# Performance work log

Measured on AMD Instinct MI355X. Metric: run time of the kernel, lower is better.

Reference implementation:

```python
import jax, jax.numpy as jnp
import numpy as np

EMBED_DIM = 768
NUM_HEADS = 12
HEAD_DIM = EMBED_DIM // NUM_HEADS // 2  # 32
MLP_DIM = 3072
DEPTH = 1
LAMBDA_INIT = 0.8 - 0.6 * float(np.exp(-0.3 * (DEPTH - 1)))  # 0.2
EPS = 1e-5


def layernorm(x, g, b):
    mu = jnp.mean(x, axis=-1, keepdims=True)
    var = jnp.mean((x - mu) ** 2, axis=-1, keepdims=True)
    return (x - mu) * jax.lax.rsqrt(var + EPS) * g + b


def rmsnorm(x, g):
    ms = jnp.mean(x ** 2, axis=-1, keepdims=True)
    return x * jax.lax.rsqrt(ms + EPS) * g


def setup_inputs() -> dict:
    key = jax.random.key(0)
    ks = jax.random.split(key, 16)
    d, m, hd = EMBED_DIM, MLP_DIM, HEAD_DIM
    inp = {
        "x": jax.random.normal(ks[0], (32, 577, d), dtype=jnp.float32),
        "ln1_g": jnp.ones((d,), jnp.float32),
        "ln1_b": jnp.zeros((d,), jnp.float32),
        "wq": jax.random.normal(ks[1], (d, d), jnp.float32) * 0.02,
        "wk": jax.random.normal(ks[2], (d, d), jnp.float32) * 0.02,
        "wv": jax.random.normal(ks[3], (d, d), jnp.float32) * 0.02,
        "wo": jax.random.normal(ks[4], (d, d), jnp.float32) * 0.02,
        "lq1": jax.random.normal(ks[5], (hd,), jnp.float32) * 0.1,
        "lk1": jax.random.normal(ks[6], (hd,), jnp.float32) * 0.1,
        "lq2": jax.random.normal(ks[7], (hd,), jnp.float32) * 0.1,
        "lk2": jax.random.normal(ks[8], (hd,), jnp.float32) * 0.1,
        "subln_g": jnp.ones((2 * hd,), jnp.float32),
        "ln2_g": jnp.ones((d,), jnp.float32),
        "ln2_b": jnp.zeros((d,), jnp.float32),
        "w1": jax.random.normal(ks[9], (m, d), jnp.float32) * 0.02,
        "b1": jnp.zeros((m,), jnp.float32),
        "w2": jax.random.normal(ks[10], (d, m), jnp.float32) * 0.02,
        "b2": jnp.zeros((d,), jnp.float32),
    }
    return inp


def diff_attn(x, wq, wk, wv, wo, lq1, lk1, lq2, lk2, subln_g):
    b, n, d = x.shape
    h, hd = NUM_HEADS, HEAD_DIM
    q = (x @ wq.T).reshape(b, n, 2 * h, hd)  # [b,n,2h,hd]
    k = (x @ wk.T).reshape(b, n, 2 * h, hd)
    v = (x @ wv.T).reshape(b, n, h, 2 * hd)  # [b,n,h,2hd]
    scale = hd ** -0.5
    scores = jnp.einsum("bnhd,bmhd->bhnm", q * scale, k)  # [b,2h,n,n]
    probs = jax.nn.softmax(scores.astype(jnp.float32), axis=-1).astype(x.dtype)
    probs = probs.reshape(b, h, 2, n, n)
    lam = jnp.exp(jnp.sum(lq1 * lk1)) - jnp.exp(jnp.sum(lq2 * lk2)) + LAMBDA_INIT
    attn = probs[:, :, 0] - lam * probs[:, :, 1]  # [b,h,n,n]
    out = jnp.einsum("bhnm,bmhe->bnhe", attn, v)  # [b,n,h,2hd]
    out = rmsnorm(out, subln_g) * (1.0 - LAMBDA_INIT)
    return out.reshape(b, n, d) @ wo.T


def reference(x, ln1_g, ln1_b, wq, wk, wv, wo, lq1, lk1, lq2, lk2, subln_g,
              ln2_g, ln2_b, w1, b1, w2, b2):
    # pre-LN -> differential attention -> residual
    a = diff_attn(layernorm(x, ln1_g, ln1_b), wq, wk, wv, wo,
                  lq1, lk1, lq2, lk2, subln_g)
    x = x + a
    # pre-LN -> GELU MLP -> residual (dropout = 0 / eval)
    h = layernorm(x, ln2_g, ln2_b)
    h = jax.nn.gelu(h @ w1.T + b1, approximate=False) @ w2.T + b2
    return x + h
```

## Files before the change

kernel.cpp:

```cpp
#include <hip/hip_runtime.h>
#include <hip/hip_bf16.h>
#include <cstdint>
#include <cstddef>

typedef __bf16 bf16_t;
typedef __attribute__((ext_vector_type(8))) __bf16 bf16x8;
typedef __attribute__((ext_vector_type(4))) __bf16 bf16x4;
typedef __attribute__((ext_vector_type(4))) float f32x4;
typedef __attribute__((ext_vector_type(4))) int int4v;
typedef __attribute__((ext_vector_type(2))) unsigned uintx2;

#define DEV static __device__ __forceinline__

#define BATCH 32
#define SEQ 577
#define DMODEL 768
#define MROWS (BATCH * SEQ)
#define MPAD 18688
#define NH 12
#define HDIM 32
#define EDIM 64
#define MLPD 3072
#define NPAD 640
#define QKVSTR 2304

DEV f32x4 mfma16(bf16x8 a, bf16x8 b, f32x4 c) {
    return __builtin_amdgcn_mfma_f32_16x16x32_bf16(a, b, c, 0, 0, 0);
}

DEV void gload16(const void* g, void* l) {
    __builtin_amdgcn_global_load_lds(
        (const __attribute__((address_space(1))) void*)(uintptr_t)g,
        (__attribute__((address_space(3))) void*)(uintptr_t)l,
        16, 0, 0);
}

DEV unsigned cvt_pk_bf16(float lo, float hi) {
    unsigned r;
    asm("v_cvt_pk_bf16_f32 %0, %1, %2" : "=v"(r) : "v"(lo), "v"(hi));
    return r;
}
DEV void plane16_swap(unsigned& a, unsigned& b) {
    asm("v_permlane16_swap_b32 %0, %1" : "+v"(a), "+v"(b));
}
DEV void plane32_swap(unsigned& a, unsigned& b) {
    asm("v_permlane32_swap_b32 %0, %1" : "+v"(a), "+v"(b));
}

DEV int xcd_swz(int orig, int nwg) {
    const int q = nwg >> 3, r = nwg & 7;
    const int xcd = orig & 7, loc = orig >> 3;
    return (xcd < r ? xcd * (q + 1) : r * (q + 1) + (xcd - r) * q) + loc;
}

__global__ __launch_bounds__(256)
void wconv_kernel(const float* __restrict__ wq, const float* __restrict__ wk,
                  const float* __restrict__ wv, const float* __restrict__ wo,
                  const float* __restrict__ w1, const float* __restrict__ w2,
                  bf16_t* __restrict__ dst)
{
    const size_t idx = ((size_t)blockIdx.x * 256 + threadIdx.x) * 4;
    const float* src;
    size_t off;
    if      (idx <  589824) { src = wq; off = idx; }
    else if (idx < 1179648) { src = wk; off = idx - 589824; }
    else if (idx < 1769472) { src = wv; off = idx - 1179648; }
    else if (idx < 2359296) { src = wo; off = idx - 1769472; }
    else if (idx < 4718592) { src = w1; off = idx - 2359296; }
    else                    { src = w2; off = idx - 4718592; }
    const f32x4 v = *(const f32x4*)&src[off];
    bf16x4 o;
#pragma unroll
    for (int u = 0; u < 4; ++u) o[u] = (bf16_t)v[u];
    *(bf16x4*)&dst[idx] = o;
}

__global__ void lam_kernel(const float* __restrict__ lq1, const float* __restrict__ lk1,
                           const float* __restrict__ lq2, const float* __restrict__ lk2,
                           float* __restrict__ lam)
{
    const int l = threadIdx.x;
    float a = 0.f, c = 0.f;
    if (l < 32) { a = lq1[l] * lk1[l]; c = lq2[l] * lk2[l]; }
#pragma unroll
    for (int m = 1; m < 32; m <<= 1) { a += __shfl_xor(a, m); c += __shfl_xor(c, m); }
    if (l == 0) *lam = expf(a) - expf(c) + 0.2f;
}

__global__ __launch_bounds__(256)
void ln_kernel(const float* __restrict__ src, const float* __restrict__ g,
               const float* __restrict__ bt, bf16_t* __restrict__ dst, const int Mv)
{
    const int row = blockIdx.x;
    const int t = threadIdx.x;
    if (row >= Mv) {
        for (int i = t; i < DMODEL; i += 256) dst[(size_t)row * DMODEL + i] = (bf16_t)0.f;
        return;
    }
    const float* p = src + (size_t)row * DMODEL;
    const float v0 = p[t], v1 = p[t + 256], v2 = p[t + 512];
    float s = v0 + v1 + v2, s2 = v0 * v0 + v1 * v1 + v2 * v2;
#pragma unroll
    for (int m = 1; m < 64; m <<= 1) { s += __shfl_xor(s, m); s2 += __shfl_xor(s2, m); }
    __shared__ float red[8];
    const int w = t >> 6;
    if ((t & 63) == 0) { red[w] = s; red[4 + w] = s2; }
    __syncthreads();
    s  = red[0] + red[1] + red[2] + red[3];
    s2 = red[4] + red[5] + red[6] + red[7];
    const float mu  = s * (1.f / DMODEL);
    const float var = s2 * (1.f / DMODEL) - mu * mu;
    const float rs = rsqrtf(var + 1e-5f);
    bf16_t* d = dst + (size_t)row * DMODEL;
    d[t      ] = (bf16_t)((v0 - mu) * rs * g[t      ] + bt[t      ]);
    d[t + 256] = (bf16_t)((v1 - mu) * rs * g[t + 256] + bt[t + 256]);
    d[t + 512] = (bf16_t)((v2 - mu) * rs * g[t + 512] + bt[t + 512]);
}

#define VM6 asm volatile("s_waitcnt vmcnt(6)" ::: "memory")
#define VM4 asm volatile("s_waitcnt vmcnt(4)" ::: "memory")
#define VM2 asm volatile("s_waitcnt vmcnt(2)" ::: "memory")
#define VM0 asm volatile("s_waitcnt vmcnt(0)" ::: "memory")
#define RAWBAR do { __builtin_amdgcn_s_barrier(); \
                    __builtin_amdgcn_sched_barrier(0); } while (0)

#define QUAD(MH, NH)                                                         \
    do {                                                                     \
        __builtin_amdgcn_s_setprio(1);                                       \
        _Pragma("unroll")                                                    \
        for (int m2_ = 0; m2_ < 4; ++m2_)                                    \
            _Pragma("unroll")                                                \
            for (int n2_ = 0; n2_ < 2; ++n2_)                                \
                _Pragma("unroll")                                            \
                for (int ks_ = 0; ks_ < 2; ++ks_)                            \
                    acc[(MH) * 4 + m2_][(NH) * 2 + n2_] =                    \
                        mfma16(af[m2_][ks_], bfr[n2_][ks_],                  \
                               acc[(MH) * 4 + m2_][(NH) * 2 + n2_]);         \
        __builtin_amdgcn_s_setprio(0);                                       \
    } while (0)

template <int EPI>
__global__ __launch_bounds__(512, 2)
void gemm8(const bf16_t* __restrict__ A, const bf16_t* __restrict__ W,
           const int K, const int N, const int NT,
           bf16_t* __restrict__ outB, float* __restrict__ outF,
           const float* __restrict__ bias, const float* __restrict__ resid,
           const int Mv)
{
    __shared__ bf16_t As[2][256 * 64];
    __shared__ bf16_t Bs[2][256 * 64];
    const int t = threadIdx.x;
    const int l = t & 63, w = t >> 6;
    const int lg = l >> 4, lc = l & 15;
    const int wr = w >> 2, wc = w & 3;

    const int nwg = gridDim.x * gridDim.y;
    const int orig = blockIdx.y * gridDim.x + blockIdx.x;
    const int wg = xcd_swz(orig, nwg);
    const int tileRow = (wg / gridDim.y) * 256;
    const int tileCol = (wg % gridDim.y) * 256;

    const int srow = t >> 3;
    const int swc = ((t & 7) ^ (srow & 7)) * 8;
    const bf16_t* pA0 = A + (size_t)(tileRow + srow) * K + swc;
    const bf16_t* pB0 = W + (size_t)(tileCol + srow) * K + swc;
    const size_t rstep = (size_t)64 * K;

    f32x4 acc[8][4];
#pragma unroll
    for (int m = 0; m < 8; ++m)
#pragma unroll
        for (int n = 0; n < 4; ++n) acc[m][n] = f32x4{0.f, 0.f, 0.f, 0.f};

    auto stA = [&](int bsel, int tk, int mh) {
        const bf16_t* s = pA0 + (size_t)tk * 64 + (size_t)mh * 128 * K;
        gload16(s,         &As[bsel][(mh * 1024 + t) * 8]);
        gload16(s + rstep, &As[bsel][(mh * 1024 + 512 + t) * 8]);
    };
    auto stB = [&](int bsel, int tk, int nh) {
        const bf16_t* s = pB0 + (size_t)tk * 64 + (size_t)nh * 128 * K;
        gload16(s,         &Bs[bsel][(nh * 1024 + t) * 8]);
        gload16(s + rstep, &Bs[bsel][(nh * 1024 + 512 + t) * 8]);
    };

    bf16x8 af[4][2], bfr[2][2];
    const int rdsw = lc & 7;
    auto rdA = [&](int bsel, int mh) {
#pragma unroll
        for (int m2 = 0; m2 < 4; ++m2)
#pragma unroll
            for (int ks = 0; ks < 2; ++ks)
                af[m2][ks] = *(const bf16x8*)&As[bsel][
                    (mh * 128 + m2 * 32 + wr * 16 + lc) * 64 + ((ks * 4 + lg) ^ rdsw) * 8];
    };
    auto rdB = [&](int bsel, int nh) {
#pragma unroll
        for (int n2 = 0; n2 < 2; ++n2)
#pragma unroll
            for (int ks = 0; ks < 2; ++ks)
                bfr[n2][ks] = *(const bf16x8*)&Bs[bsel][
                    (nh * 128 + n2 * 64 + wc * 16 + lc) * 64 + ((ks * 4 + lg) ^ rdsw) * 8];
    };

    stA(0, 0, 0);
    stB(0, 0, 0);
    stB(0, 0, 1);
    stA(0, 0, 1);

#pragma unroll 1
    for (int kt = 0; kt < NT - 1; ++kt) {
        const int bs = kt & 1, bn = bs ^ 1;
        stA(bn, kt + 1, 0); VM6; RAWBAR;
        rdA(bs, 0); rdB(bs, 0); QUAD(0, 0);
        stB(bn, kt + 1, 0); VM6; RAWBAR;
        rdB(bs, 1); QUAD(0, 1);
        stB(bn, kt + 1, 1); VM6; RAWBAR;
        rdA(bs, 1); QUAD(1, 1);
        stA(bn, kt + 1, 1);
        rdB(bs, 0); QUAD(1, 0);
    }
    {
        const int bs = (NT - 1) & 1;
        VM4; RAWBAR;
        rdA(bs, 0); rdB(bs, 0); QUAD(0, 0);
        VM2; RAWBAR;
        rdB(bs, 1); QUAD(0, 1);
        VM0; RAWBAR;
        rdA(bs, 1); QUAD(1, 1);
        rdB(bs, 0); QUAD(1, 0);
    }

#pragma unroll
    for (int m = 0; m < 8; ++m) {
        const int row0 = tileRow + (m >> 2) * 128 + (m & 3) * 32 + wr * 16 + 4 * lg;
#pragma unroll
        for (int n = 0; n < 4; ++n) {
            const int col = tileCol + (n >> 1) * 128 + (n & 1) * 64 + wc * 16 + lc;
#pragma unroll
            for (int r = 0; r < 4; ++r) {
                const int row = row0 + r;
                float v = acc[m][n][r];
                if (EPI == 0) {
                    outB[(size_t)row * N + col] = (bf16_t)v;
                } else if (EPI == 1) {
                    const float xin = (row < Mv) ? resid[(size_t)row * N + col] : 0.f;
                    outF[(size_t)row * N + col] = v + xin;
                } else if (EPI == 2) {
                    v += bias[col];
                    v = 0.5f * v * (1.f + erff(v * 0.70710678118654752f));
                    outB[(size_t)row * N + col] = (bf16_t)v;
                } else {
                    if (row < Mv)
                        outF[(size_t)row * N + col] = v + bias[col] + resid[(size_t)row * N + col];
                }
            }
        }
    }
}

__global__ __launch_bounds__(256)
void vtrans_kernel(const bf16_t* __restrict__ qkv, bf16_t* __restrict__ vt)
{
    const int nt = blockIdx.x, h = blockIdx.y, b = blockIdx.z;
    const int t = threadIdx.x;
    __shared__ bf16_t T[64][72];
    {
        const int nl = t >> 2, e0 = (t & 3) * 16;
        const int n = nt * 64 + nl;
        bf16x8 a, c;
        if (n < SEQ) {
            const bf16_t* src = &qkv[((size_t)b * SEQ + n) * QKVSTR + 1536 + h * EDIM + e0];
            a = *(const bf16x8*)src;
            c = *(const bf16x8*)(src + 8);
        } else {
#pragma unroll
            for (int u = 0; u < 8; ++u) { a[u] = (bf16_t)0.f; c[u] = (bf16_t)0.f; }
        }
#pragma unroll
        for (int u = 0; u < 8; ++u) { T[e0 + u][nl] = a[u]; T[e0 + 8 + u][nl] = c[u]; }
    }
    __syncthreads();
    {
        const int e = t >> 2, n0 = (t & 3) * 16;
        bf16x8 a, c;
#pragma unroll
        for (int u = 0; u < 8; ++u) { a[u] = T[e][n0 + u]; c[u] = T[e][n0 + 8 + u]; }
        bf16_t* d = &vt[((size_t)(b * NH + h) * EDIM + e) * NPAD + nt * 64 + n0];
        *(bf16x8*)d = a;
        *(bf16x8*)(d + 8) = c;
    }
}

__global__ __launch_bounds__(256)
void attn_kernel(const bf16_t* __restrict__ qkv, const bf16_t* __restrict__ vtp,
                 const float* __restrict__ lamp, const float* __restrict__ subg,
                 bf16_t* __restrict__ outp)
{
    const int orig = blockIdx.x + 10 * (blockIdx.y + 12 * blockIdx.z);
    const int wg = xcd_swz(orig, 3840);
    const int qt = wg % 10;
    const int h  = (wg / 10) % 12;
    const int b  = wg / 120;
    const int t = threadIdx.x, w = t >> 6, l = t & 63;
    const int lg = l >> 4, lc = l & 15;
    const float lam = *lamp;
    const float SC2 = 0.25503487f;
    const float MARG = 8.0f * 0.25503487f;

    __shared__ bf16_t Ks[2][64 * 64];
    __shared__ bf16_t Vs[2][64 * 64];

    const size_t mb = (size_t)b * SEQ;
    const int q0row = qt * 64 + w * 16;

    bf16x8 qf[2];
#pragma unroll
    for (int hh = 0; hh < 2; ++hh)
        qf[hh] = *(const bf16x8*)&qkv[(mb + q0row + lc) * QKVSTR
                                      + h * 64 + hh * 32 + 8 * lg];

    f32x4 O[2][4];
    f32x4 Ol[2];
#pragma unroll
    for (int hh = 0; hh < 2; ++hh) {
        Ol[hh] = f32x4{0.f, 0.f, 0.f, 0.f};
#pragma unroll
        for (int ef = 0; ef < 4; ++ef) O[hh][ef] = f32x4{0.f, 0.f, 0.f, 0.f};
    }

    bf16x8 ones;
#pragma unroll
    for (int u = 0; u < 8; ++u) ones[u] = (bf16_t)1.0f;

    const int r0 = t >> 3, c0 = (t & 7);
    const int r1 = r0 + 32;
    const bf16_t* kg0 = &qkv[(mb + r0) * QKVSTR + 768 + h * 64 + ((c0 ^ (r0 & 7)) * 8)];
    const bf16_t* kg1 = &qkv[(mb + r1) * QKVSTR + 768 + h * 64 + ((c0 ^ (r1 & 7)) * 8)];
    const bf16_t* vg0 = &vtp[(size_t)((b * NH + h) * EDIM + r0) * NPAD + ((c0 ^ (r0 & 7)) * 8)];
    const bf16_t* vg1 = &vtp[(size_t)((b * NH + h) * EDIM + r1) * NPAD + ((c0 ^ (r1 & 7)) * 8)];

    auto stage = [&](int kt, int bufi) {
        gload16(kg0 + (size_t)kt * (64 * QKVSTR), &Ks[bufi][t * 8]);
        gload16(kg1 + (size_t)kt * (64 * QKVSTR), &Ks[bufi][(t + 256) * 8]);
        gload16(vg0 + kt * 64, &Vs[bufi][t * 8]);
        gload16(vg1 + kt * 64, &Vs[bufi][(t + 256) * 8]);
    };

    stage(0, 0);
    int buf = 0;

    const int swz = lc & 7;
    int koff[2], voff[2];
#pragma unroll
    for (int hh = 0; hh < 2; ++hh) koff[hh] = lc * 64 + (((hh * 4 + lg) ^ swz) * 8);
#pragma unroll
    for (int ks = 0; ks < 2; ++ks) voff[ks] = lc * 64 + (((ks * 4 + lg) ^ swz) * 8);

#pragma unroll 1
    for (int kt = 0; kt < 10; ++kt) {
        __builtin_amdgcn_s_barrier();
        if (kt < 9) {
            stage(kt + 1, buf ^ 1);
            VM4;
        } else {
            VM0;
        }
        __builtin_amdgcn_s_barrier();
        __builtin_amdgcn_sched_barrier(0);

        const bf16_t* Kb = &Ks[buf][0];
        const bf16_t* Vb = &Vs[buf][0];

#pragma unroll
        for (int hh = 0; hh < 2; ++hh) {
            bf16x8 kf[4];
#pragma unroll
            for (int f = 0; f < 4; ++f)
                kf[f] = *(const bf16x8*)&Kb[koff[hh] + f * 1024];
            f32x4 s[4];
#pragma unroll
            for (int f = 0; f < 4; ++f)
                s[f] = mfma16(kf[f], qf[hh], f32x4{0.f, 0.f, 0.f, 0.f});
            if (kt == 9) {
#pragma unroll
                for (int f = 0; f < 4; ++f)
#pragma unroll
                    for (int r = 0; r < 4; ++r)
                        if (f | r) s[f][r] = -3e38f;
                if (lg != 0) s[0][0] = -3e38f;
            }
            unsigned wd[4][2];
#pragma unroll
            for (int f = 0; f < 4; ++f) {
                float p0 = __builtin_amdgcn_exp2f(__builtin_fmaf(s[f][0], SC2, -MARG));
                float p1 = __builtin_amdgcn_exp2f(__builtin_fmaf(s[f][1], SC2, -MARG));
                float p2 = __builtin_amdgcn_exp2f(__builtin_fmaf(s[f][2], SC2, -MARG));
                float p3 = __builtin_amdgcn_exp2f(__builtin_fmaf(s[f][3], SC2, -MARG));
                wd[f][0] = cvt_pk_bf16(p0, p1);
                wd[f][1] = cvt_pk_bf16(p2, p3);
            }
#pragma unroll
            for (int half = 0; half < 2; ++half) {
#pragma unroll
                for (int p = 0; p < 2; ++p) {
                    unsigned& Aa = wd[half * 2][p];
                    unsigned& Bb = wd[half * 2 + 1][p];
                    plane32_swap(Aa, Bb);
                    plane16_swap(Aa, Bb);
                }
            }
            const bf16x8 pa0 = __builtin_bit_cast(bf16x8,
                int4v{(int)wd[0][0], (int)wd[0][1], (int)wd[1][0], (int)wd[1][1]});
            const bf16x8 pa1 = __builtin_bit_cast(bf16x8,
                int4v{(int)wd[2][0], (int)wd[2][1], (int)wd[3][0], (int)wd[3][1]});

#pragma unroll
            for (int ef = 0; ef < 4; ++ef) {
                const bf16x8 vb0 = *(const bf16x8*)&Vb[voff[0] + ef * 1024];
                const bf16x8 vb1 = *(const bf16x8*)&Vb[voff[1] + ef * 1024];
                O[hh][ef] = mfma16(vb0, pa0, O[hh][ef]);
                O[hh][ef] = mfma16(vb1, pa1, O[hh][ef]);
            }
            Ol[hh] = mfma16(ones, pa0, Ol[hh]);
            Ol[hh] = mfma16(ones, pa1, Ol[hh]);
        }
        buf ^= 1;
    }

    {
        const float i0 = 1.f / Ol[0][0];
        const float i1 = lam / Ol[1][0];
        float comb[4][4];
        float ms = 0.f;
#pragma unroll
        for (int ef = 0; ef < 4; ++ef)
#pragma unroll
            for (int r = 0; r < 4; ++r) {
                const float o = O[0][ef][r] * i0 - O[1][ef][r] * i1;
                comb[ef][r] = o;
                ms += o * o;
            }
        ms += __shfl_xor(ms, 16);
        ms += __shfl_xor(ms, 32);
        const float sc = rsqrtf(ms * (1.f / 64.f) + 1e-5f) * 0.8f;
        const int nq = q0row + lc;
        if (nq < SEQ) {
            bf16_t* dst = &outp[(mb + nq) * DMODEL + h * EDIM + 4 * lg];
#pragma unroll
            for (int ef = 0; ef < 4; ++ef) {
                const f32x4 g4 = *(const f32x4*)&subg[ef * 16 + 4 * lg];
                const unsigned u0 = cvt_pk_bf16(comb[ef][0] * sc * g4[0],
                                                comb[ef][1] * sc * g4[1]);
                const unsigned u1 = cvt_pk_bf16(comb[ef][2] * sc * g4[2],
                                                comb[ef][3] * sc * g4[3]);
                *(uintx2*)(dst + ef * 16) = uintx2{u0, u1};
            }
        }
    }
}

extern "C" void kernel_launch(void* const* d_in, const int* in_sizes, int n_in,
                              void* d_out, int out_size, void* d_ws, size_t ws_size,
                              hipStream_t stream)
{
    const float* x    = (const float*)d_in[0];
    const float* ln1g = (const float*)d_in[1];
    const float* ln1b = (const float*)d_in[2];
    const float* wq   = (const float*)d_in[3];
    const float* wk   = (const float*)d_in[4];
    const float* wv   = (const float*)d_in[5];
    const float* wo   = (const float*)d_in[6];
    const float* lq1  = (const float*)d_in[7];
    const float* lk1  = (const float*)d_in[8];
    const float* lq2  = (const float*)d_in[9];
    const float* lk2  = (const float*)d_in[10];
    const float* subg = (const float*)d_in[11];
    const float* ln2g = (const float*)d_in[12];
    const float* ln2b = (const float*)d_in[13];
    const float* w1   = (const float*)d_in[14];
    const float* b1   = (const float*)d_in[15];
    const float* w2   = (const float*)d_in[16];
    const float* b2   = (const float*)d_in[17];

    char* ws = (char*)d_ws;
    bf16_t* wAll = (bf16_t*)ws;
    bf16_t* wob = wAll + 1769472;
    bf16_t* w1b = wAll + 2359296;
    bf16_t* w2b = wAll + 4718592;
    ws += 7077888ull * 2;
    float* lamP = (float*)ws; ws += 256;
    bf16_t* xn   = (bf16_t*)ws; ws += (size_t)MPAD * DMODEL * 2;
    bf16_t* qkvb = (bf16_t*)ws;
    bf16_t* h1   = qkvb;
    ws += (size_t)MPAD * QKVSTR * 2;
    bf16_t* vtb  = (bf16_t*)ws; ws += (size_t)(BATCH * NH) * EDIM * NPAD * 2;
    bf16_t* aout = (bf16_t*)ws; ws += (size_t)MPAD * DMODEL * 2;
    float* x1    = (float*)ws;  ws += (size_t)MPAD * DMODEL * 4;

    wconv_kernel<<<6912, 256, 0, stream>>>(wq, wk, wv, wo, w1, w2, wAll);
    lam_kernel<<<1, 64, 0, stream>>>(lq1, lk1, lq2, lk2, lamP);
    ln_kernel<<<MPAD, 256, 0, stream>>>(x, ln1g, ln1b, xn, MROWS);

    gemm8<0><<<dim3(73, 9), 512, 0, stream>>>(xn, wAll, 768, QKVSTR, 12,
                                              qkvb, nullptr, nullptr, nullptr, MROWS);

    vtrans_kernel<<<dim3(10, 12, 32), 256, 0, stream>>>(qkvb, vtb);
    attn_kernel<<<dim3(10, 12, 32), 256, 0, stream>>>(qkvb, vtb, lamP, subg, aout);

    gemm8<1><<<dim3(73, 3), 512, 0, stream>>>(aout, wob, 768, 768, 12,
                                              nullptr, x1, nullptr, x, MROWS);
    ln_kernel<<<MPAD, 256, 0, stream>>>(x1, ln2g, ln2b, xn, MROWS);
    gemm8<2><<<dim3(73, 12), 512, 0, stream>>>(xn, w1b, 768, MLPD, 12,
                                               h1, nullptr, b1, nullptr, MROWS);
    gemm8<3><<<dim3(73, 3), 512, 0, stream>>>(h1, w2b, MLPD, 768, 48,
                                              nullptr, (float*)d_out, b2, x1, MROWS);
}
```

Measured before the change: 604.0 us.

## Restructure GEMM main loop into 8-wave ping-pong schedule with separate B fragment registers

The GEMM k-loop is rescheduled so LDS fragment reads and the next tile's global loads are issued before a barrier, then MFMA quads run between barriers, in a ping-pong style. B fragments are split into two register sets (b0r, b1r) so the first-half B fragment can be reused for the last quad without re-reading LDS. The cost targeted is LDS read latency and redundant B reads exposed before MFMAs. In exchange it adds more barriers per iteration and more register pressure, which may hurt occupancy at launch bounds 512x2.

Result: no change. 600.9 us (-0.5%).

```diff
diff --git a/kernel.cpp b/kernel.cpp
--- a/kernel.cpp
+++ b/kernel.cpp
@@ -117,14 +117,13 @@
     d[t + 512] = (bf16_t)((v2 - mu) * rs * g[t + 512] + bt[t + 512]);
 }
 
-#define VM6 asm volatile("s_waitcnt vmcnt(6)" ::: "memory")
 #define VM4 asm volatile("s_waitcnt vmcnt(4)" ::: "memory")
 #define VM2 asm volatile("s_waitcnt vmcnt(2)" ::: "memory")
 #define VM0 asm volatile("s_waitcnt vmcnt(0)" ::: "memory")
-#define RAWBAR do { __builtin_amdgcn_s_barrier(); \
-                    __builtin_amdgcn_sched_barrier(0); } while (0)
-
-#define QUAD(MH, NH)                                                         \
+#define SB0 __builtin_amdgcn_sched_barrier(0)
+#define BAR __builtin_amdgcn_s_barrier()
+
+#define QUAD(MH, BFR, NHh)                                                   \
     do {                                                                     \
         __builtin_amdgcn_s_setprio(1);                                       \
         _Pragma("unroll")                                                    \
@@ -133,9 +132,9 @@
             for (int n2_ = 0; n2_ < 2; ++n2_)                                \
                 _Pragma("unroll")                                            \
                 for (int ks_ = 0; ks_ < 2; ++ks_)                            \
-                    acc[(MH) * 4 + m2_][(NH) * 2 + n2_] =                    \
-                        mfma16(af[m2_][ks_], bfr[n2_][ks_],                  \
-                               acc[(MH) * 4 + m2_][(NH) * 2 + n2_]);         \
+                    acc[(MH) * 4 + m2_][(NHh) * 2 + n2_] =                   \
+                        mfma16(af[m2_][ks_], BFR[n2_][ks_],                  \
+                               acc[(MH) * 4 + m2_][(NHh) * 2 + n2_]);        \
         __builtin_amdgcn_s_setprio(0);                                       \
     } while (0)
 
@@ -183,7 +182,7 @@
         gload16(s + rstep, &Bs[bsel][(nh * 1024 + 512 + t) * 8]);
     };
 
-    bf16x8 af[4][2], bfr[2][2];
+    bf16x8 af[4][2], b0r[2][2], b1r[2][2];
     const int rdsw = lc & 7;
     auto rdA = [&](int bsel, int mh) {
 #pragma unroll
@@ -193,41 +192,67 @@
                 af[m2][ks] = *(const bf16x8*)&As[bsel][
                     (mh * 128 + m2 * 32 + wr * 16 + lc) * 64 + ((ks * 4 + lg) ^ rdsw) * 8];
     };
-    auto rdB = [&](int bsel, int nh) {
+    auto rdB0 = [&](int bsel) {
 #pragma unroll
         for (int n2 = 0; n2 < 2; ++n2)
 #pragma unroll
             for (int ks = 0; ks < 2; ++ks)
-                bfr[n2][ks] = *(const bf16x8*)&Bs[bsel][
-                    (nh * 128 + n2 * 64 + wc * 16 + lc) * 64 + ((ks * 4 + lg) ^ rdsw) * 8];
+                b0r[n2][ks] = *(const bf16x8*)&Bs[bsel][
+                    (n2 * 64 + wc * 16 + lc) * 64 + ((ks * 4 + lg) ^ rdsw) * 8];
+    };
+    auto rdB1 = [&](int bsel) {
+#pragma unroll
+        for (int n2 = 0; n2 < 2; ++n2)
+#pragma unroll
+            for (int ks = 0; ks < 2; ++ks)
+                b1r[n2][ks] = *(const bf16x8*)&Bs[bsel][
+                    (128 + n2 * 64 + wc * 16 + lc) * 64 + ((ks * 4 + lg) ^ rdsw) * 8];
     };
 
     stA(0, 0, 0);
     stB(0, 0, 0);
     stB(0, 0, 1);
     stA(0, 0, 1);
+    VM4; BAR;
 
 #pragma unroll 1
     for (int kt = 0; kt < NT - 1; ++kt) {
         const int bs = kt & 1, bn = bs ^ 1;
-        stA(bn, kt + 1, 0); VM6; RAWBAR;
-        rdA(bs, 0); rdB(bs, 0); QUAD(0, 0);
-        stB(bn, kt + 1, 0); VM6; RAWBAR;
-        rdB(bs, 1); QUAD(0, 1);
-        stB(bn, kt + 1, 1); VM6; RAWBAR;
-        rdA(bs, 1); QUAD(1, 1);
+        rdA(bs, 0); rdB0(bs);
+        stA(bn, kt + 1, 0);
+        SB0; VM4; BAR; SB0;
+        QUAD(0, b0r, 0);
+        BAR;
+        rdB1(bs);
+        stB(bn, kt + 1, 0);
+        SB0; VM4; BAR; SB0;
+        QUAD(0, b1r, 1);
+        BAR;
+        rdA(bs, 1);
+        stB(bn, kt + 1, 1);
+        SB0; BAR; SB0;
+        QUAD(1, b1r, 1);
+        BAR;
         stA(bn, kt + 1, 1);
-        rdB(bs, 0); QUAD(1, 0);
-    }
+        SB0; VM4; BAR; SB0;
+        QUAD(1, b0r, 0);
+        BAR;
+    }
+
     {
         const int bs = (NT - 1) & 1;
-        VM4; RAWBAR;
-        rdA(bs, 0); rdB(bs, 0); QUAD(0, 0);
-        VM2; RAWBAR;
-        rdB(bs, 1); QUAD(0, 1);
-        VM0; RAWBAR;
-        rdA(bs, 1); QUAD(1, 1);
-        rdB(bs, 0); QUAD(1, 0);
+        rdA(bs, 0); rdB0(bs);
+        SB0; VM2; BAR; SB0;
+        QUAD(0, b0r, 0);
+        BAR;
+        rdB1(bs);
+        SB0; VM0; BAR; SB0;
+        QUAD(0, b1r, 1);
+        BAR;
+        rdA(bs, 1);
+        SB0; BAR; SB0;
+        QUAD(1, b1r, 1);
+        QUAD(1, b0r, 0);
     }
 
 #pragma unroll
```

## Replace 256x256 GEMM with 128x256 tile, K=32 triple-buffered pipeline

Applied to the files above, without the earlier changes.

The GEMM kernel moves from 256x256 tiles with K=64 double buffering to 128x256 tiles with K=32 and a three-stage LDS ring. Loads for step k+2 are issued while computing step k, and launch bounds allow four blocks per CU instead of two. The smaller tiles double the grid and raise occupancy, which should hide memory latency better and reduce wave quantization. In exchange, each tile reuses its operands less, so global and LDS traffic per FLOP rises and more barriers run per K step.

Measured after the change: 559.1 us. 7.4% less time.

```diff
diff --git a/kernel.cpp b/kernel.cpp
--- a/kernel.cpp
+++ b/kernel.cpp
@@ -117,38 +117,36 @@
     d[t + 512] = (bf16_t)((v2 - mu) * rs * g[t + 512] + bt[t + 512]);
 }
 
-#define VM6 asm volatile("s_waitcnt vmcnt(6)" ::: "memory")
-#define VM4 asm volatile("s_waitcnt vmcnt(4)" ::: "memory")
-#define VM2 asm volatile("s_waitcnt vmcnt(2)" ::: "memory")
+#define VM3 asm volatile("s_waitcnt vmcnt(3)" ::: "memory")
 #define VM0 asm volatile("s_waitcnt vmcnt(0)" ::: "memory")
-#define RAWBAR do { __builtin_amdgcn_s_barrier(); \
-                    __builtin_amdgcn_sched_barrier(0); } while (0)
-
-#define QUAD(MH, NH)                                                         \
+#define SB0 __builtin_amdgcn_sched_barrier(0)
+#define BAR __builtin_amdgcn_s_barrier()
+
+#define ASZ 4096
+#define BSZ 8192
+
+#define QUAD8(H, BP)                                                         \
     do {                                                                     \
         __builtin_amdgcn_s_setprio(1);                                       \
         _Pragma("unroll")                                                    \
         for (int m2_ = 0; m2_ < 4; ++m2_)                                    \
             _Pragma("unroll")                                                \
-            for (int n2_ = 0; n2_ < 2; ++n2_)                                \
-                _Pragma("unroll")                                            \
-                for (int ks_ = 0; ks_ < 2; ++ks_)                            \
-                    acc[(MH) * 4 + m2_][(NH) * 2 + n2_] =                    \
-                        mfma16(af[m2_][ks_], bfr[n2_][ks_],                  \
-                               acc[(MH) * 4 + m2_][(NH) * 2 + n2_]);         \
+            for (int j_ = 0; j_ < 2; ++j_)                                   \
+                acc[m2_][(H) * 2 + j_] =                                     \
+                    mfma16(af[m2_], BP[j_], acc[m2_][(H) * 2 + j_]);         \
         __builtin_amdgcn_s_setprio(0);                                       \
     } while (0)
 
 template <int EPI>
-__global__ __launch_bounds__(512, 2)
-void gemm8(const bf16_t* __restrict__ A, const bf16_t* __restrict__ W,
+__global__ __launch_bounds__(512, 4)
+void gemm4(const bf16_t* __restrict__ A, const bf16_t* __restrict__ W,
            const int K, const int N, const int NT,
            bf16_t* __restrict__ outB, float* __restrict__ outF,
            const float* __restrict__ bias, const float* __restrict__ resid,
            const int Mv)
 {
-    __shared__ bf16_t As[2][256 * 64];
-    __shared__ bf16_t Bs[2][256 * 64];
+    __shared__ bf16_t As[3 * ASZ];
+    __shared__ bf16_t Bs[3 * BSZ];
     const int t = threadIdx.x;
     const int l = t & 63, w = t >> 6;
     const int lg = l >> 4, lc = l & 15;
@@ -157,85 +155,77 @@
     const int nwg = gridDim.x * gridDim.y;
     const int orig = blockIdx.y * gridDim.x + blockIdx.x;
     const int wg = xcd_swz(orig, nwg);
-    const int tileRow = (wg / gridDim.y) * 256;
+    const int tileRow = (wg / gridDim.y) * 128;
     const int tileCol = (wg % gridDim.y) * 256;
 
-    const int srow = t >> 3;
-    const int swc = ((t & 7) ^ (srow & 7)) * 8;
-    const bf16_t* pA0 = A + (size_t)(tileRow + srow) * K + swc;
-    const bf16_t* pB0 = W + (size_t)(tileCol + srow) * K + swc;
-    const size_t rstep = (size_t)64 * K;
-
-    f32x4 acc[8][4];
-#pragma unroll
-    for (int m = 0; m < 8; ++m)
+    const int srow = t >> 2;
+    const int csrc = ((t & 3) ^ ((t >> 3) & 3)) * 8;
+    const bf16_t* srcA  = A + (size_t)(tileRow + srow) * K + csrc;
+    const bf16_t* srcB0 = W + (size_t)(tileCol + srow) * K + csrc;
+    const bf16_t* srcB1 = W + (size_t)(tileCol + 128 + srow) * K + csrc;
+
+    f32x4 acc[4][4];
+#pragma unroll
+    for (int m = 0; m < 4; ++m)
 #pragma unroll
         for (int n = 0; n < 4; ++n) acc[m][n] = f32x4{0.f, 0.f, 0.f, 0.f};
 
-    auto stA = [&](int bsel, int tk, int mh) {
-        const bf16_t* s = pA0 + (size_t)tk * 64 + (size_t)mh * 128 * K;
-        gload16(s,         &As[bsel][(mh * 1024 + t) * 8]);
-        gload16(s + rstep, &As[bsel][(mh * 1024 + 512 + t) * 8]);
+    const int rch = (lg ^ ((lc >> 1) & 3)) * 8;
+    const int aoff = (wr * 64 + lc) * 32 + rch;
+    const int boff = (wc * 64 + lc) * 32 + rch;
+
+    bf16x8 af[4], b01[2], b23[2];
+
+    auto stageA = [&](int kt, bf16_t* dst) {
+        gload16(srcA + (size_t)kt * 32, dst + t * 8);
     };
-    auto stB = [&](int bsel, int tk, int nh) {
-        const bf16_t* s = pB0 + (size_t)tk * 64 + (size_t)nh * 128 * K;
-        gload16(s,         &Bs[bsel][(nh * 1024 + t) * 8]);
-        gload16(s + rstep, &Bs[bsel][(nh * 1024 + 512 + t) * 8]);
+    auto stageB = [&](int kt, bf16_t* dst) {
+        gload16(srcB0 + (size_t)kt * 32, dst + t * 8);
+        gload16(srcB1 + (size_t)kt * 32, dst + (t + 512) * 8);
     };
-
-    bf16x8 af[4][2], bfr[2][2];
-    const int rdsw = lc & 7;
-    auto rdA = [&](int bsel, int mh) {
+    auto rdA = [&](const bf16_t* buf) {
 #pragma unroll
         for (int m2 = 0; m2 < 4; ++m2)
-#pragma unroll
-            for (int ks = 0; ks < 2; ++ks)
-                af[m2][ks] = *(const bf16x8*)&As[bsel][
-                    (mh * 128 + m2 * 32 + wr * 16 + lc) * 64 + ((ks * 4 + lg) ^ rdsw) * 8];
+            af[m2] = *(const bf16x8*)&buf[aoff + m2 * 512];
     };
-    auto rdB = [&](int bsel, int nh) {
-#pragma unroll
-        for (int n2 = 0; n2 < 2; ++n2)
-#pragma unroll
-            for (int ks = 0; ks < 2; ++ks)
-                bfr[n2][ks] = *(const bf16x8*)&Bs[bsel][
-                    (nh * 128 + n2 * 64 + wc * 16 + lc) * 64 + ((ks * 4 + lg) ^ rdsw) * 8];
+    auto rdB = [&](const bf16_t* buf, int h, bf16x8* bp) {
+#pragma unroll
+        for (int j = 0; j < 2; ++j)
+            bp[j] = *(const bf16x8*)&buf[boff + (h * 2 + j) * 512];
     };
 
-    stA(0, 0, 0);
-    stB(0, 0, 0);
-    stB(0, 0, 1);
-    stA(0, 0, 1);
+    auto STEP = [&](int kt, const bf16_t* AsR, const bf16_t* BsR,
+                    bf16_t* AsS, bf16_t* BsS) {
+        rdA(AsR); rdB(BsR, 0, b01);
+        if (kt + 2 < NT) stageA(kt + 2, AsS);
+        SB0; BAR; SB0;
+        QUAD8(0, b01);
+        BAR;
+        rdB(BsR, 1, b23);
+        if (kt + 2 < NT) stageB(kt + 2, BsS);
+        if (kt == NT - 2) { VM0; } else if (kt < NT - 2) { VM3; }
+        SB0; BAR; SB0;
+        QUAD8(1, b23);
+        BAR;
+    };
+
+    stageA(0, As);          stageB(0, Bs);
+    stageA(1, As + ASZ);    stageB(1, Bs + BSZ);
+    VM3; BAR;
 
 #pragma unroll 1
-    for (int kt = 0; kt < NT - 1; ++kt) {
-        const int bs = kt & 1, bn = bs ^ 1;
-        stA(bn, kt + 1, 0); VM6; RAWBAR;
-        rdA(bs, 0); rdB(bs, 0); QUAD(0, 0);
-        stB(bn, kt + 1, 0); VM6; RAWBAR;
-        rdB(bs, 1); QUAD(0, 1);
-        stB(bn, kt + 1, 1); VM6; RAWBAR;
-        rdA(bs, 1); QUAD(1, 1);
-        stA(bn, kt + 1, 1);
-        rdB(bs, 0); QUAD(1, 0);
-    }
-    {
-        const int bs = (NT - 1) & 1;
-        VM4; RAWBAR;
-        rdA(bs, 0); rdB(bs, 0); QUAD(0, 0);
-        VM2; RAWBAR;
-        rdB(bs, 1); QUAD(0, 1);
-        VM0; RAWBAR;
-        rdA(bs, 1); QUAD(1, 1);
-        rdB(bs, 0); QUAD(1, 0);
-    }
-
-#pragma unroll
-    for (int m = 0; m < 8; ++m) {
-        const int row0 = tileRow + (m >> 2) * 128 + (m & 3) * 32 + wr * 16 + 4 * lg;
+    for (int kt = 0; kt < NT; kt += 3) {
+        STEP(kt,     As,           Bs,           As + 2 * ASZ, Bs + 2 * BSZ);
+        STEP(kt + 1, As + ASZ,     Bs + BSZ,     As,           Bs);
+        STEP(kt + 2, As + 2 * ASZ, Bs + 2 * BSZ, As + ASZ,     Bs + BSZ);
+    }
+
+#pragma unroll
+    for (int m = 0; m < 4; ++m) {
+        const int row0 = tileRow + wr * 64 + m * 16 + 4 * lg;
 #pragma unroll
         for (int n = 0; n < 4; ++n) {
-            const int col = tileCol + (n >> 1) * 128 + (n & 1) * 64 + wc * 16 + lc;
+            const int col = tileCol + wc * 64 + n * 16 + lc;
 #pragma unroll
             for (int r = 0; r < 4; ++r) {
                 const int row = row0 + r;
@@ -361,7 +351,7 @@
         __builtin_amdgcn_s_barrier();
         if (kt < 9) {
             stage(kt + 1, buf ^ 1);
-            VM4;
+            asm volatile("s_waitcnt vmcnt(4)" ::: "memory");
         } else {
             VM0;
         }
@@ -501,17 +491,17 @@
     lam_kernel<<<1, 64, 0, stream>>>(lq1, lk1, lq2, lk2, lamP);
     ln_kernel<<<MPAD, 256, 0, stream>>>(x, ln1g, ln1b, xn, MROWS);
 
-    gemm8<0><<<dim3(73, 9), 512, 0, stream>>>(xn, wAll, 768, QKVSTR, 12,
-                                              qkvb, nullptr, nullptr, nullptr, MROWS);
+    gemm4<0><<<dim3(146, 9), 512, 0, stream>>>(xn, wAll, 768, QKVSTR, 24,
+                                               qkvb, nullptr, nullptr, nullptr, MROWS);
 
     vtrans_kernel<<<dim3(10, 12, 32), 256, 0, stream>>>(qkvb, vtb);
     attn_kernel<<<dim3(10, 12, 32), 256, 0, stream>>>(qkvb, vtb, lamP, subg, aout);
 
-    gemm8<1><<<dim3(73, 3), 512, 0, stream>>>(aout, wob, 768, 768, 12,
-                                              nullptr, x1, nullptr, x, MROWS);
+    gemm4<1><<<dim3(146, 3), 512, 0, stream>>>(aout, wob, 768, 768, 24,
+                                               nullptr, x1, nullptr, x, MROWS);
     ln_kernel<<<MPAD, 256, 0, stream>>>(x1, ln2g, ln2b, xn, MROWS);
-    gemm8<2><<<dim3(73, 12), 512, 0, stream>>>(xn, w1b, 768, MLPD, 12,
-                                               h1, nullptr, b1, nullptr, MROWS);
-    gemm8<3><<<dim3(73, 3), 512, 0, stream>>>(h1, w2b, MLPD, 768, 48,
-                                              nullptr, (float*)d_out, b2, x1, MROWS);
-}
+    gemm4<2><<<dim3(146, 12), 512, 0, stream>>>(xn, w1b, 768, MLPD, 24,
+                                                h1, nullptr, b1, nullptr, MROWS);
+    gemm4<3><<<dim3(146, 3), 512, 0, stream>>>(h1, w2b, MLPD, 768, 96,
+                                               nullptr, (float*)d_out, b2, x1, MROWS);
+}
```
